# Performance work log

Hardware: AMD Instinct MI355X
Metric: run time of the kernel (lower is better)

The kernel has to match this reference:

```python
import jax, jax.numpy as jnp
import numpy as np

B, S, NH, HD = 2, 2048, 32, 128     # batch seqs, tokens per seq, heads, head_dim
H = NH * HD                          # hidden = 4096
BLOCK = 64                           # paged KV-cache block size
NBLK = S // BLOCK                    # blocks per sequence
NUM_BLOCKS = B * NBLK                # total cache blocks


def alibi_slopes(n):
    # n is a power of two: slope_i = 2^(-8*(i+1)/n)
    return np.asarray([2.0 ** (-8.0 * (i + 1) / n) for i in range(n)], dtype=np.float32)


def setup_inputs() -> dict:
    key = jax.random.key(0)
    k1, k2, k3 = jax.random.split(key, 3)
    hidden_states = jax.random.normal(k1, (B * S, H), jnp.float32)
    w_pack = jax.random.normal(k2, (H, 3 * H), jnp.float32) * 0.02
    o_proj_w = jax.random.normal(k3, (H, H), jnp.float32) * 0.02
    k_cache = jnp.zeros((NUM_BLOCKS, BLOCK, NH, HD), jnp.float32)
    v_cache = jnp.zeros((NUM_BLOCKS, BLOCK, NH, HD), jnp.float32)
    block_offsets = jnp.arange(NUM_BLOCKS, dtype=jnp.int32).reshape(B, NBLK)
    return {
        "hidden_states": hidden_states,
        "w_pack": w_pack,
        "o_proj_w": o_proj_w,
        "k_cache": k_cache,
        "v_cache": v_cache,
        "block_offsets": block_offsets,
    }


def reference(hidden_states, w_pack, o_proj_w, k_cache, v_cache, block_offsets):
    # fused QKV projection, chunk(3, -1)
    qkv = hidden_states @ w_pack                      # [B*S, 3H]
    q, k, v = jnp.split(qkv, 3, axis=-1)
    q = q.reshape(B, S, NH, HD)
    k = k.reshape(B, NBLK, BLOCK, NH, HD)
    v = v.reshape(B, NBLK, BLOCK, NH, HD)

    # fill_kv_cache: scatter new K/V into paged cache blocks
    k_cache = k_cache.at[block_offsets].set(k)        # [NUM_BLOCKS, BLOCK, NH, HD]
    v_cache = v_cache.at[block_offsets].set(v)

    # paged read: gather non-contiguous blocks back per sequence
    kg = k_cache[block_offsets].reshape(B, S, NH, HD)
    vg = v_cache[block_offsets].reshape(B, S, NH, HD)

    slopes = jnp.asarray(alibi_slopes(NH))            # [NH]
    scale = 1.0 / jnp.sqrt(jnp.float32(HD))
    scores = jnp.einsum('bqhd,bkhd->bhqk', q, kg) * scale   # [B,NH,S,S]
    pos = jnp.arange(S)
    # ALiBi bias: slope * key_position (row-shift invariant under softmax)
    scores = scores + slopes[None, :, None, None] * pos[None, None, None, :]
    causal = pos[:, None] >= pos[None, :]             # [S,S]
    scores = jnp.where(causal[None, None], scores, jnp.float32(-1e30))
    probs = jax.nn.softmax(scores, axis=-1)
    attn = jnp.einsum('bhqk,bkhd->bqhd', probs, vg).reshape(B * S, H)
    return attn @ o_proj_w
```

## Files before the change

### kernel.cpp

```cpp
#include <hip/hip_runtime.h>
#include <hip/hip_bf16.h>
#include <stdint.h>

typedef __attribute__((ext_vector_type(4))) float f32x4;
typedef __attribute__((ext_vector_type(8))) __bf16 bf16x8;
typedef __attribute__((ext_vector_type(8))) unsigned short u16x8;
typedef __attribute__((ext_vector_type(4))) unsigned short u16x4;
typedef __attribute__((ext_vector_type(4))) unsigned int u32x4;

#define GLL16(g, l) __builtin_amdgcn_global_load_lds( \
    (const __attribute__((address_space(1))) unsigned int*)(uintptr_t)(g), \
    (__attribute__((address_space(3))) unsigned int*)(uintptr_t)(l), 16, 0, 0)

__device__ __forceinline__ unsigned short bf16u(float f) {
  return __builtin_bit_cast(unsigned short, __float2bfloat16(f));
}

#define PB 2
#define PS 2048
#define PNH 32
#define PHD 128
#define PH 4096
#define P3H 12288

__global__ __launch_bounds__(256)
void cvt_f32_bf16(const float* __restrict__ in, unsigned short* __restrict__ out, int n) {
  int stride = gridDim.x * blockDim.x;
  for (int i = blockIdx.x * blockDim.x + threadIdx.x; i * 8 < n; i += stride) {
    int base = i * 8;
    f32x4 a = *(const f32x4*)(in + base);
    f32x4 b = *(const f32x4*)(in + base + 4);
    u16x8 o;
#pragma unroll
    for (int j = 0; j < 4; ++j) { o[j] = bf16u(a[j]); o[4 + j] = bf16u(b[j]); }
    *(u16x8*)(out + base) = o;
  }
}

__global__ __launch_bounds__(256)
void transpose_cvt(const float* __restrict__ in, unsigned short* __restrict__ out,
                   int K, int N) {
  __shared__ __align__(16) unsigned short tile[64][68];
  int k0 = blockIdx.y * 64, n0 = blockIdx.x * 64;
  int t = threadIdx.x;
  int rr = t >> 4, cc = (t & 15) * 4;
#pragma unroll
  for (int p = 0; p < 4; ++p) {
    int r = rr + p * 16;
    f32x4 v = *(const f32x4*)(in + (size_t)(k0 + r) * N + n0 + cc);
    u16x4 w;
#pragma unroll
    for (int j = 0; j < 4; ++j) w[j] = bf16u(v[j]);
    *(u16x4*)&tile[r][cc] = w;
  }
  __syncthreads();
#pragma unroll
  for (int p = 0; p < 4; ++p) {
    int nl = rr + p * 16;
    u16x4 w;
#pragma unroll
    for (int j = 0; j < 4; ++j) w[j] = tile[cc + j][nl];
    *(u16x4*)(out + (size_t)(n0 + nl) * K + k0 + cc) = w;
  }
}

#define STAGEHT(T, OP, H) do { \
    const unsigned short* s_ = (OP) ? bS : aS; \
    char* d_ = smem + (((T) & 1) << 16) + ((OP) << 15) + ((H) << 14) + (wave << 10); \
    GLL16(s_ + ((size_t)((H) << 7)) * K + (size_t)(T) * 64, d_); \
    GLL16(s_ + ((size_t)(((H) << 7) + 64)) * K + (size_t)(T) * 64, d_ + 8192); \
  } while (0)

#define RD_AV8(RI, BUFA) do { \
    _Pragma("unroll") \
    for (int i_ = 0; i_ < 4; ++i_) { \
      av[2 * i_]     = *(const bf16x8*)((BUFA) + ((RI) << 13) + (i_ << 11) + (lr << 7) + ch0); \
      av[2 * i_ + 1] = *(const bf16x8*)((BUFA) + ((RI) << 13) + (i_ << 11) + (lr << 7) + (ch0 ^ 64)); \
    } } while (0)

#define RD_BV4(CI, BUFB, DST) do { \
    _Pragma("unroll") \
    for (int j_ = 0; j_ < 2; ++j_) { \
      DST[2 * j_]     = *(const bf16x8*)((BUFB) + ((CI) << 12) + (j_ << 11) + (lr << 7) + ch0); \
      DST[2 * j_ + 1] = *(const bf16x8*)((BUFB) + ((CI) << 12) + (j_ << 11) + (lr << 7) + (ch0 ^ 64)); \
    } } while (0)

#define MFMA16(RI, CI, BV) do { \
    _Pragma("unroll") \
    for (int i_ = 0; i_ < 4; ++i_) \
      _Pragma("unroll") \
      for (int j_ = 0; j_ < 2; ++j_) { \
        acc[(RI) * 4 + i_][(CI) * 2 + j_] = __builtin_amdgcn_mfma_f32_16x16x32_bf16(av[2 * i_],     BV[2 * j_],     acc[(RI) * 4 + i_][(CI) * 2 + j_], 0, 0, 0); \
        acc[(RI) * 4 + i_][(CI) * 2 + j_] = __builtin_amdgcn_mfma_f32_16x16x32_bf16(av[2 * i_ + 1], BV[2 * j_ + 1], acc[(RI) * 4 + i_][(CI) * 2 + j_], 0, 0, 0); \
      } } while (0)

#define TILE8(T, S1, S3, S4, VM) do { \
    char* bufA_ = smem + (((T) & 1) << 16) + (wm << 14); \
    char* bufB_ = smem + (((T) & 1) << 16) + 32768 + ((wn >> 1) << 14) + ((wn & 1) << 13); \
     \
    RD_AV8(0, bufA_); \
    RD_BV4(0, bufB_, bv0); \
    if (S1) STAGEHT((T) + 1, 1, 1); \
    __builtin_amdgcn_s_barrier(); \
    asm volatile("s_waitcnt lgkmcnt(0)" ::: "memory"); \
    __builtin_amdgcn_s_setprio(1); MFMA16(0, 0, bv0); __builtin_amdgcn_s_setprio(0); \
    __builtin_amdgcn_s_barrier(); \
     \
    RD_BV4(1, bufB_, bv1); \
    __builtin_amdgcn_s_barrier(); \
    asm volatile("s_waitcnt lgkmcnt(0)" ::: "memory"); \
    __builtin_amdgcn_s_setprio(1); MFMA16(0, 1, bv1); __builtin_amdgcn_s_setprio(0); \
    __builtin_amdgcn_s_barrier(); \
     \
    RD_AV8(1, bufA_); \
    if (S3) STAGEHT((T) + 2, 1, 0); \
    __builtin_amdgcn_s_barrier(); \
    asm volatile("s_waitcnt lgkmcnt(0)" ::: "memory"); \
    __builtin_amdgcn_s_setprio(1); MFMA16(1, 0, bv0); __builtin_amdgcn_s_setprio(0); \
    __builtin_amdgcn_s_barrier(); \
     \
    if (S4) { STAGEHT((T) + 2, 0, 0); STAGEHT((T) + 2, 0, 1); } \
    __builtin_amdgcn_s_barrier(); \
    __builtin_amdgcn_s_setprio(1); MFMA16(1, 1, bv1); __builtin_amdgcn_s_setprio(0); \
    if ((VM) == 6)      asm volatile("s_waitcnt vmcnt(6)" ::: "memory"); \
    else if ((VM) == 0) asm volatile("s_waitcnt vmcnt(0)" ::: "memory"); \
    __builtin_amdgcn_s_barrier(); \
  } while (0)

template<int OUTF32>
__global__ __launch_bounds__(512, 2)
void gemm256(const unsigned short* __restrict__ A, const unsigned short* __restrict__ Bt,
             void* __restrict__ Cv, int M, int N, int K) {
  __shared__ __align__(16) char smem[131072];
  const int tid = threadIdx.x;
  const int wave = tid >> 6, lane = tid & 63;
  const int lr = lane & 15, lg = lane >> 4;
  const int wm = wave >> 2, wn = wave & 3;
  const int ch0 = ((lg ^ (lr & 7)) << 4);
  const int nbn = N >> 8;
  const int nbm = M >> 8;
  int bid = blockIdx.x;
  const int bnx = nbn >> 3;
  int x = bid & 7;
  int l = bid >> 3;
  int bm = l % nbm;
  int bn = x * bnx + l / nbm;
  const size_t arow = (size_t)bm << 8;
  const size_t brow = (size_t)bn << 8;

  const int sg = lane >> 3;
  const int scolE = ((lane & 7) ^ sg) << 3;
  const unsigned short* aS = A  + (arow + (wave << 3) + sg) * (size_t)K + scolE;
  const unsigned short* bS = Bt + (brow + (wave << 3) + sg) * (size_t)K + scolE;

  f32x4 acc[8][4] = {};
  bf16x8 av[8], bv0[4], bv1[4];

  STAGEHT(0, 0, 0); STAGEHT(0, 0, 1); STAGEHT(0, 1, 0); STAGEHT(0, 1, 1);
  STAGEHT(1, 1, 0); STAGEHT(1, 0, 0); STAGEHT(1, 0, 1);
  asm volatile("s_waitcnt vmcnt(6)" ::: "memory");
  __builtin_amdgcn_s_barrier();

  for (int t = 0; t < 62; ++t) TILE8(t, 1, 1, 1, 6);
  TILE8(62, 1, 0, 0, 0);
  TILE8(63, 0, 0, 0, -1);

  int crow = (bm << 8) + (wm << 7) + (lg << 2);
  int ccol = (bn << 8) + (wn << 6) + lr;
#pragma unroll
  for (int i = 0; i < 8; ++i)
#pragma unroll
    for (int j = 0; j < 4; ++j)
#pragma unroll
      for (int r = 0; r < 4; ++r) {
        size_t off = (size_t)(crow + (i << 4) + r) * N + ccol + (j << 4);
        if (OUTF32) ((float*)Cv)[off] = acc[i][j][r];
        else        ((unsigned short*)Cv)[off] = bf16u(acc[i][j][r]);
      }
}

__global__ __launch_bounds__(512, 2)
void attn_kernel(const unsigned short* __restrict__ qkv, unsigned short* __restrict__ out) {
  __shared__ __align__(16) unsigned short Ks[2][64 * 128];
  __shared__ __align__(16) unsigned short Vt[128 * 64];
  __shared__ __align__(16) unsigned short Ps[8][32 * 72];
  int tid = threadIdx.x, wave = tid >> 6, lane = tid & 63;
  int lr = lane & 15, lg = lane >> 4;
  int idx = blockIdx.x;
  int qtsel = idx & 7, h = (idx >> 3) & 31, bsel = idx >> 8;
  int qt = bsel ? qtsel : 7 - qtsel;
  size_t rb = (size_t)bsel * PS;
  int qcol = h << 7, kcol = PH + (h << 7), vcol = 2 * PH + (h << 7);
  int q0 = (qt << 8) + (wave << 5);

  bf16x8 aq[2][4];
#pragma unroll
  for (int qs = 0; qs < 2; ++qs)
#pragma unroll
    for (int f = 0; f < 4; ++f)
      aq[qs][f] = *(const bf16x8*)(qkv + (rb + q0 + (qs << 4) + lr) * P3H + qcol + (f << 5) + (lg << 3));

  float m_run[2][4], l_run[2][4];
#pragma unroll
  for (int qs = 0; qs < 2; ++qs)
#pragma unroll
    for (int r = 0; r < 4; ++r) { m_run[qs][r] = -1e30f; l_run[qs][r] = 0.f; }
  f32x4 acc_o[2][8] = {};

  float slope2 = __builtin_amdgcn_exp2f(-(float)(h + 1) * 0.25f) * 1.44269504f;
  const float scale2 = 0.08838834764831845f * 1.44269504f;

  char* KsB = (char*)Ks;
  char* VtB = (char*)Vt;
  const int kk0 = (tid & 31) << 1;
  const int d0 = (tid >> 5) << 3;

  {
    size_t krow = rb;
#pragma unroll
    for (int i = 0; i < 2; ++i) {
      int pf = (wave << 11) | (i << 10) | (lane << 4);
      int row = pf >> 8;
      int lch = ((pf >> 4) & 15) ^ (row & 7);
      GLL16(qkv + (krow + row) * P3H + kcol + (lch << 3), KsB + (wave << 11) + (i << 10));
    }
  }
  u32x4 vr0 = *(const u32x4*)(qkv + (rb + kk0 + 0) * P3H + vcol + d0);
  u32x4 vr1 = *(const u32x4*)(qkv + (rb + kk0 + 1) * P3H + vcol + d0);

  const int tmax = 4 * qt + 3;
  for (int t = 0; t <= tmax; ++t) {
    int cur = t & 1;
    char* KsCur = KsB + (cur << 14);
    char* KsNxt = KsB + ((cur ^ 1) << 14);
    bool more = (t < tmax);

    u32x4 nv0 = {}, nv1 = {};
    if (more) {
      size_t krow = rb + ((size_t)(t + 1) << 6);
#pragma unroll
      for (int i = 0; i < 2; ++i) {
        int pf = (wave << 11) | (i << 10) | (lane << 4);
        int row = pf >> 8;
        int lch = ((pf >> 4) & 15) ^ (row & 7);
        GLL16(qkv + (krow + row) * P3H + kcol + (lch << 3), KsNxt + (wave << 11) + (i << 10));
      }
      nv0 = *(const u32x4*)(qkv + (krow + kk0 + 0) * P3H + vcol + d0);
      nv1 = *(const u32x4*)(qkv + (krow + kk0 + 1) * P3H + vcol + d0);
    }

    if (more) asm volatile("s_waitcnt vmcnt(4)" ::: "memory");
    else      asm volatile("s_waitcnt vmcnt(0)" ::: "memory");

    {
      const unsigned short* e0 = (const unsigned short*)&vr0;
      const unsigned short* e1 = (const unsigned short*)&vr1;
#pragma unroll
      for (int j = 0; j < 8; ++j) {
        int d = d0 + j;
        unsigned int w = (unsigned int)e0[j] | ((unsigned int)e1[j] << 16);
        int byteoff = ((d << 7) + (kk0 << 1)) ^ ((d & 7) << 4);
        *(unsigned int*)(VtB + byteoff) = w;
      }
    }
    asm volatile("s_waitcnt lgkmcnt(0)" ::: "memory");
    __builtin_amdgcn_s_barrier();

    f32x4 sc[2][4];
    __builtin_amdgcn_s_setprio(1);
#pragma unroll
    for (int f = 0; f < 4; ++f) {
      f32x4 c0 = {}, c1 = {};
#pragma unroll
      for (int ks = 0; ks < 4; ++ks) {
        int kkr = (f << 4) + lr;
        int ch = (lg + (ks << 2)) ^ (kkr & 7);
        bf16x8 bk = *(const bf16x8*)(KsCur + (kkr << 8) + (ch << 4));
        c0 = __builtin_amdgcn_mfma_f32_16x16x32_bf16(aq[0][ks], bk, c0, 0, 0, 0);
        c1 = __builtin_amdgcn_mfma_f32_16x16x32_bf16(aq[1][ks], bk, c1, 0, 0, 0);
      }
      sc[0][f] = c0; sc[1][f] = c1;
    }
    __builtin_amdgcn_s_setprio(0);

    int kvb = t << 6;
    bool needmask = (kvb + 63 > q0);
#pragma unroll
    for (int qs = 0; qs < 2; ++qs) {
      float vals[4][4];
#pragma unroll
      for (int f = 0; f < 4; ++f) {
        int kv = kvb + (f << 4) + lr;
        float bias = slope2 * (float)kv;
#pragma unroll
        for (int r = 0; r < 4; ++r) {
          float v = sc[qs][f][r] * scale2 + bias;
          if (needmask && kv > q0 + (qs << 4) + (lg << 2) + r) v = -1e30f;
          vals[r][f] = v;
        }
      }
      float alpha[4];
#pragma unroll
      for (int r = 0; r < 4; ++r) {
        float mr = fmaxf(fmaxf(vals[r][0], vals[r][1]), fmaxf(vals[r][2], vals[r][3]));
#pragma unroll
        for (int d2 = 1; d2 < 16; d2 <<= 1) mr = fmaxf(mr, __shfl_xor(mr, d2, 16));
        float mnew = fmaxf(m_run[qs][r], mr);
        alpha[r] = __builtin_amdgcn_exp2f(m_run[qs][r] - mnew);
        m_run[qs][r] = mnew;
      }
#pragma unroll
      for (int r = 0; r < 4; ++r) {
        float s = 0.f;
#pragma unroll
        for (int f = 0; f < 4; ++f) {
          float p = __builtin_amdgcn_exp2f(vals[r][f] - m_run[qs][r]);
          s += p;
          Ps[wave][((qs << 4) + (lg << 2) + r) * 72 + (f << 4) + lr] = bf16u(p);
        }
        l_run[qs][r] = l_run[qs][r] * alpha[r] + s;
      }
#pragma unroll
      for (int d = 0; d < 8; ++d) {
        f32x4 a4 = acc_o[qs][d];
#pragma unroll
        for (int r = 0; r < 4; ++r) a4[r] *= alpha[r];
        acc_o[qs][d] = a4;
      }
    }

    bf16x8 pa[2][2];
#pragma unroll
    for (int qs = 0; qs < 2; ++qs)
#pragma unroll
      for (int ks = 0; ks < 2; ++ks)
        pa[qs][ks] = *(const bf16x8*)((char*)&Ps[wave][0] + ((qs << 4) + lr) * 144 + (ks << 6) + (lg << 4));
    __builtin_amdgcn_s_setprio(1);
#pragma unroll
    for (int d = 0; d < 8; ++d) {
#pragma unroll
      for (int ks = 0; ks < 2; ++ks) {
        int dr = (d << 4) + lr;
        int ch = (lg + (ks << 2)) ^ (dr & 7);
        bf16x8 bv = *(const bf16x8*)(VtB + (dr << 7) + (ch << 4));
        acc_o[0][d] = __builtin_amdgcn_mfma_f32_16x16x32_bf16(pa[0][ks], bv, acc_o[0][d], 0, 0, 0);
        acc_o[1][d] = __builtin_amdgcn_mfma_f32_16x16x32_bf16(pa[1][ks], bv, acc_o[1][d], 0, 0, 0);
      }
    }
    __builtin_amdgcn_s_setprio(0);
    __builtin_amdgcn_s_barrier();

    if (more) { vr0 = nv0; vr1 = nv1; }
  }

#pragma unroll
  for (int qs = 0; qs < 2; ++qs) {
    float rinv[4];
#pragma unroll
    for (int r = 0; r < 4; ++r) {
      float s = l_run[qs][r];
#pragma unroll
      for (int d2 = 1; d2 < 16; d2 <<= 1) s += __shfl_xor(s, d2, 16);
      rinv[r] = 1.f / s;
    }
#pragma unroll
    for (int d = 0; d < 8; ++d)
#pragma unroll
      for (int r = 0; r < 4; ++r) {
        float o = acc_o[qs][d][r] * rinv[r];
        out[(rb + q0 + (qs << 4) + (lg << 2) + r) * PH + (h << 7) + (d << 4) + lr] = bf16u(o);
      }
  }
}

extern "C" void kernel_launch(void* const* d_in, const int* in_sizes, int n_in,
                              void* d_out, int out_size, void* d_ws, size_t ws_size,
                              hipStream_t stream) {
  const float* hidden = (const float*)d_in[0];
  const float* w_pack = (const float*)d_in[1];
  const float* o_proj = (const float*)d_in[2];

  char* ws = (char*)d_ws;
  unsigned short* wpackT = (unsigned short*)(ws);
  unsigned short* qkv    = (unsigned short*)(ws + 100663296);
  unsigned short* oprojT = (unsigned short*)(ws + 201326592);
  unsigned short* hbf    = (unsigned short*)(ws + 234881024);
  unsigned short* attnb  = hbf;

  int M = PB * PS;

  cvt_f32_bf16<<<2048, 256, 0, stream>>>(hidden, hbf, M * PH);
  transpose_cvt<<<dim3(P3H / 64, PH / 64), 256, 0, stream>>>(w_pack, wpackT, PH, P3H);
  transpose_cvt<<<dim3(PH / 64, PH / 64), 256, 0, stream>>>(o_proj, oprojT, PH, PH);
  gemm256<0><<<(M / 256) * (P3H / 256), 512, 0, stream>>>(hbf, wpackT, qkv, M, P3H, PH);
  attn_kernel<<<PB * PNH * (PS / 256), 512, 0, stream>>>(qkv, attnb);
  gemm256<1><<<(M / 256) * (PH / 256), 512, 0, stream>>>(attnb, oprojT, d_out, M, PH, PH);
}
```

Measured before the change: 710.1 us.

## Add 4-stage pipelined GEMM with register double-buffering for QKV projection

Adds a new 256x256 bf16 GEMM kernel that uses a four-deep LDS ring of 32-wide K slices, prefetching three tiles ahead with direct global-to-LDS loads. A-fragments are double-buffered in registers so LDS reads for the next tile overlap the MFMAs of the current one. The kernel uses a single barrier per tile and sched_group_barrier hints to interleave reads, loads and MFMAs. It replaces the old 8-phase kernel only for the QKV projection; the output projection keeps the renamed original. This costs more registers and relies on exact vmcnt accounting being correct.

```diff
diff --git a/kernel.cpp b/kernel.cpp
--- a/kernel.cpp
+++ b/kernel.cpp
@@ -64,6 +64,108 @@
   }
 }
 
+#define GLLP(TT, P) do { int sb_ = ((TT) & 3) << 15; \
+    const unsigned short* s_ = (P) == 0 ? aSrc0 : (P) == 1 ? aSrc1 : (P) == 2 ? bSrc0 : bSrc1; \
+    GLL16(s_ + (size_t)(TT) * 32, smem + sb_ + ((P) << 13) + (wave << 10)); } while (0)
+
+#define RD_AV(DST, BUFP, I) DST[I] = *(const bf16x8*)((BUFP) + (((wm << 7) + ((I) << 4) + lr) << 6) + lchunk)
+#define RD_BV(DST, BUFP, J) DST[J] = *(const bf16x8*)((BUFP) + 16384 + (((wn << 6) + ((J) << 4) + lr) << 6) + lchunk)
+
+#define SGB __builtin_amdgcn_sched_group_barrier
+
+#define TILE(TC, AC, AN, DOSTAGE, DOREAD, VM, DOBAR) do { \
+    char* nA_ = smem + ((((TC) + 1) & 3) << 15); \
+    __builtin_amdgcn_s_setprio(1); \
+    _Pragma("unroll") \
+    for (int g = 0; g < 4; ++g) { \
+      if (DOREAD) { RD_AV(AN, nA_, 2 * g); RD_AV(AN, nA_, 2 * g + 1); } \
+      if (DOSTAGE) GLLP((TC) + 3, g); \
+      _Pragma("unroll") \
+      for (int i = 2 * g; i < 2 * g + 2; ++i) \
+        _Pragma("unroll") \
+        for (int j = 0; j < 4; ++j) \
+          acc[i][j] = __builtin_amdgcn_mfma_f32_16x16x32_bf16(AC[i], bvv[j], acc[i][j], 0, 0, 0); \
+      SGB(0x100, 2, 0); SGB(0x020, 1, 0); SGB(0x008, 8, 0); \
+    } \
+    if (DOREAD) { RD_BV(bvv, nA_, 0); RD_BV(bvv, nA_, 1); RD_BV(bvv, nA_, 2); RD_BV(bvv, nA_, 3); } \
+    __builtin_amdgcn_s_setprio(0); \
+    if ((VM) == 4)      asm volatile("s_waitcnt vmcnt(4)" ::: "memory"); \
+    else if ((VM) == 0) asm volatile("s_waitcnt vmcnt(0)" ::: "memory"); \
+    if (DOBAR) __builtin_amdgcn_s_barrier(); \
+  } while (0)
+
+template<int OUTF32>
+__global__ __launch_bounds__(512, 2)
+void gemm_r14(const unsigned short* __restrict__ A, const unsigned short* __restrict__ Bt,
+              void* __restrict__ Cv, int M, int N, int K) {
+  __shared__ __align__(16) char smem[131072];
+  const int tid = threadIdx.x;
+  const int wave = tid >> 6, lane = tid & 63;
+  const int lr = lane & 15, lg = lane >> 4;
+  const int wm = wave >> 2, wn = wave & 3;
+  const int lchunk = (lg ^ ((lr >> 1) & 3)) << 4;
+  const int nbn = N >> 8;
+  const int nbm = M >> 8;
+  int bid = blockIdx.x;
+  const int bnx = nbn >> 3;
+  int x = bid & 7;
+  int l = bid >> 3;
+  int bm = l % nbm;
+  int bn = x * bnx + l / nbm;
+  const size_t arow = (size_t)bm << 8;
+  const size_t brow = (size_t)bn << 8;
+
+  const int srow = (wave << 4) + (lane >> 2);
+  const int scol = ((lane & 3) ^ ((lane >> 3) & 3)) << 3;
+  const unsigned short* aSrc0 = A  + (arow + srow) * K + scol;
+  const unsigned short* aSrc1 = A  + (arow + 128 + srow) * K + scol;
+  const unsigned short* bSrc0 = Bt + (brow + srow) * K + scol;
+  const unsigned short* bSrc1 = Bt + (brow + 128 + srow) * K + scol;
+
+  f32x4 acc[8][4] = {};
+
+#pragma unroll
+  for (int p = 0; p < 4; ++p) GLLP(0, p);
+#pragma unroll
+  for (int p = 0; p < 4; ++p) GLLP(1, p);
+#pragma unroll
+  for (int p = 0; p < 4; ++p) GLLP(2, p);
+  asm volatile("s_waitcnt vmcnt(4)" ::: "memory");
+  __builtin_amdgcn_s_barrier();
+
+  bf16x8 avA[8], avB[8], bvv[4];
+  {
+    char* b0 = smem;
+#pragma unroll
+    for (int i = 0; i < 8; ++i) RD_AV(avA, b0, i);
+#pragma unroll
+    for (int j = 0; j < 4; ++j) RD_BV(bvv, b0, j);
+  }
+
+  for (int p = 0; p < 62; ++p) {
+    int t = 2 * p;
+    TILE(t,     avA, avB, 1, 1, 4, 1);
+    TILE(t + 1, avB, avA, 1, 1, 4, 1);
+  }
+  TILE(124, avA, avB, 1, 1, 4, 1);
+  TILE(125, avB, avA, 0, 1, 0, 1);
+  TILE(126, avA, avB, 0, 1, -1, 0);
+  TILE(127, avB, avA, 0, 0, -1, 0);
+
+  int crow = (bm << 8) + (wm << 7) + (lg << 2);
+  int ccol = (bn << 8) + (wn << 6) + lr;
+#pragma unroll
+  for (int i = 0; i < 8; ++i)
+#pragma unroll
+    for (int j = 0; j < 4; ++j)
+#pragma unroll
+      for (int r = 0; r < 4; ++r) {
+        size_t off = (size_t)(crow + (i << 4) + r) * N + ccol + (j << 4);
+        if (OUTF32) ((float*)Cv)[off] = acc[i][j][r];
+        else        ((unsigned short*)Cv)[off] = bf16u(acc[i][j][r]);
+      }
+}
+
 #define STAGEHT(T, OP, H) do { \
     const unsigned short* s_ = (OP) ? bS : aS; \
     char* d_ = smem + (((T) & 1) << 16) + ((OP) << 15) + ((H) << 14) + (wave << 10); \
@@ -97,7 +199,6 @@
 #define TILE8(T, S1, S3, S4, VM) do { \
     char* bufA_ = smem + (((T) & 1) << 16) + (wm << 14); \
     char* bufB_ = smem + (((T) & 1) << 16) + 32768 + ((wn >> 1) << 14) + ((wn & 1) << 13); \
-     \
     RD_AV8(0, bufA_); \
     RD_BV4(0, bufB_, bv0); \
     if (S1) STAGEHT((T) + 1, 1, 1); \
@@ -105,20 +206,17 @@
     asm volatile("s_waitcnt lgkmcnt(0)" ::: "memory"); \
     __builtin_amdgcn_s_setprio(1); MFMA16(0, 0, bv0); __builtin_amdgcn_s_setprio(0); \
     __builtin_amdgcn_s_barrier(); \
-     \
     RD_BV4(1, bufB_, bv1); \
     __builtin_amdgcn_s_barrier(); \
     asm volatile("s_waitcnt lgkmcnt(0)" ::: "memory"); \
     __builtin_amdgcn_s_setprio(1); MFMA16(0, 1, bv1); __builtin_amdgcn_s_setprio(0); \
     __builtin_amdgcn_s_barrier(); \
-     \
     RD_AV8(1, bufA_); \
     if (S3) STAGEHT((T) + 2, 1, 0); \
     __builtin_amdgcn_s_barrier(); \
     asm volatile("s_waitcnt lgkmcnt(0)" ::: "memory"); \
     __builtin_amdgcn_s_setprio(1); MFMA16(1, 0, bv0); __builtin_amdgcn_s_setprio(0); \
     __builtin_amdgcn_s_barrier(); \
-     \
     if (S4) { STAGEHT((T) + 2, 0, 0); STAGEHT((T) + 2, 0, 1); } \
     __builtin_amdgcn_s_barrier(); \
     __builtin_amdgcn_s_setprio(1); MFMA16(1, 1, bv1); __builtin_amdgcn_s_setprio(0); \
@@ -129,7 +227,7 @@
 
 template<int OUTF32>
 __global__ __launch_bounds__(512, 2)
-void gemm256(const unsigned short* __restrict__ A, const unsigned short* __restrict__ Bt,
+void gemm_8p(const unsigned short* __restrict__ A, const unsigned short* __restrict__ Bt,
              void* __restrict__ Cv, int M, int N, int K) {
   __shared__ __align__(16) char smem[131072];
   const int tid = threadIdx.x;
@@ -392,7 +490,7 @@
   cvt_f32_bf16<<<2048, 256, 0, stream>>>(hidden, hbf, M * PH);
   transpose_cvt<<<dim3(P3H / 64, PH / 64), 256, 0, stream>>>(w_pack, wpackT, PH, P3H);
   transpose_cvt<<<dim3(PH / 64, PH / 64), 256, 0, stream>>>(o_proj, oprojT, PH, PH);
-  gemm256<0><<<(M / 256) * (P3H / 256), 512, 0, stream>>>(hbf, wpackT, qkv, M, P3H, PH);
+  gemm_r14<0><<<(M / 256) * (P3H / 256), 512, 0, stream>>>(hbf, wpackT, qkv, M, P3H, PH);
   attn_kernel<<<PB * PNH * (PS / 256), 512, 0, stream>>>(qkv, attnb);
-  gemm256<1><<<(M / 256) * (PH / 256), 512, 0, stream>>>(attnb, oprojT, d_out, M, PH, PH);
-}
+  gemm_8p<1><<<(M / 256) * (PH / 256), 512, 0, stream>>>(attnb, oprojT, d_out, M, PH, PH);
+}
```

Result: slower. 737.6 us (+3.9%).
